# Kernel tuning notes

Measured on AMD Instinct MI355X. Metric: run time of the kernel, lower is better.

Reference implementation:

```python
import jax, jax.numpy as jnp
import numpy as np

H = 128
N_CAN = 100000
N_FLAG = 50000
E = 600000
L = 500000


def _sage_conv(x_src, x_dst, edge_index, Wl, bl, Wr):
    # PyG SAGEConv (mean aggr): lin_l(mean_{j in N(i)} x_j) + lin_r(x_i)
    src, dst = edge_index[0], edge_index[1]
    msg = x_src[src]                                        # [E, H] gather
    n_dst = x_dst.shape[0]
    agg = jax.ops.segment_sum(msg, dst, num_segments=n_dst)  # [N_dst, H]
    cnt = jax.ops.segment_sum(jnp.ones((msg.shape[0],), msg.dtype), dst,
                              num_segments=n_dst)
    mean = agg / jnp.maximum(cnt, 1.0)[:, None]
    return mean @ Wl.T + bl + x_dst @ Wr.T


def setup_inputs() -> dict:
    key = jax.random.key(0)
    ks = jax.random.split(key, 16)
    s = 1.0 / np.sqrt(H)
    inp = {
        'can_node_id': jnp.arange(N_CAN, dtype=jnp.int64) if jax.config.jax_enable_x64 else jnp.arange(N_CAN, dtype=jnp.int32),
        'flag_node_id': jnp.arange(N_FLAG, dtype=jnp.int32),
        'edge_index_cf': jnp.stack([
            jax.random.randint(ks[0], (E,), 0, N_CAN),
            jax.random.randint(ks[1], (E,), 0, N_FLAG)]),
        'edge_index_fc': jnp.stack([
            jax.random.randint(ks[2], (E,), 0, N_FLAG),
            jax.random.randint(ks[3], (E,), 0, N_CAN)]),
        'edge_label_index': jnp.stack([
            jax.random.randint(ks[4], (L,), 0, N_CAN),
            jax.random.randint(ks[5], (L,), 0, N_FLAG)]),
        'can_emb': jax.random.normal(ks[6], (N_CAN, H), jnp.float32),
        'flag_emb': jax.random.normal(ks[7], (N_FLAG, H), jnp.float32),
        # SAGEConv for edge type CAN->flag (updates flag nodes)
        'Wl_cf': jax.random.normal(ks[8], (H, H), jnp.float32) * s,
        'bl_cf': jnp.zeros((H,), jnp.float32),
        'Wr_cf': jax.random.normal(ks[9], (H, H), jnp.float32) * s,
        # SAGEConv for edge type flag->CAN (updates CAN nodes)
        'Wl_fc': jax.random.normal(ks[10], (H, H), jnp.float32) * s,
        'bl_fc': jnp.zeros((H,), jnp.float32),
        'Wr_fc': jax.random.normal(ks[11], (H, H), jnp.float32) * s,
        # classifier MLP
        'W1': jax.random.normal(ks[12], (H, 2 * H), jnp.float32) * (1.0 / np.sqrt(2 * H)),
        'b1': jnp.zeros((H,), jnp.float32),
        'W2': jax.random.normal(ks[13], (1, H), jnp.float32) * s,
        'b2': jnp.zeros((1,), jnp.float32),
    }
    return inp


def reference(can_node_id, flag_node_id, edge_index_cf, edge_index_fc,
              edge_label_index, can_emb, flag_emb,
              Wl_cf, bl_cf, Wr_cf, Wl_fc, bl_fc, Wr_fc,
              W1, b1, W2, b2):
    # embedding lookups
    x_can = can_emb[can_node_id]    # [N_CAN, H]
    x_flag = flag_emb[flag_node_id]  # [N_FLAG, H]
    # to_hetero single SAGE layer + relu (dropout is identity in eval)
    upd_flag = jax.nn.relu(_sage_conv(x_can, x_flag, edge_index_cf, Wl_cf, bl_cf, Wr_cf))
    upd_can = jax.nn.relu(_sage_conv(x_flag, x_can, edge_index_fc, Wl_fc, bl_fc, Wr_fc))
    # link prediction classifier
    src = upd_can[edge_label_index[0]]   # [L, H]
    dst = upd_flag[edge_label_index[1]]  # [L, H]
    h = jax.nn.relu(jnp.concatenate([src, dst], axis=-1) @ W1.T + b1)
    out = h @ W2.T + b2
    return out.reshape(-1)
```

## Files before the change

kernel.cpp:

```cpp
#include <hip/hip_runtime.h>
#include <hip/hip_bf16.h>

#define H 128
#define BSH 8
#define MAXB 1024

typedef __attribute__((ext_vector_type(8))) short short8;
typedef __attribute__((ext_vector_type(4))) short short4v;
typedef __attribute__((ext_vector_type(4))) float floatx4;
typedef unsigned short ushort_t;
typedef unsigned int uint_t;

__device__ __forceinline__ short f2bf(float f) {
    __hip_bfloat16 h = __float2bfloat16(f);
    return *reinterpret_cast<short*>(&h);
}
__device__ __forceinline__ float bflo(uint_t u) { return __uint_as_float(u << 16); }
__device__ __forceinline__ float bfhi(uint_t u) { return __uint_as_float(u & 0xFFFF0000u); }
__device__ __forceinline__ uint_t pack_bf2(float x, float y) {
    return (uint_t)(ushort_t)f2bf(x) | ((uint_t)(ushort_t)f2bf(y) << 16);
}

__global__ __launch_bounds__(256)
void bucket_hist_cvt_kernel(const int* __restrict__ ei1, const int* __restrict__ ei2,
                            int E, int NF, int B, int* __restrict__ bcnt, int nbh,
                            const float* __restrict__ a, int n4a,
                            const float* __restrict__ b, int n4b,
                            ushort_t* __restrict__ da, ushort_t* __restrict__ db,
                            const float* __restrict__ Wl_cf, const float* __restrict__ Wr_cf,
                            const float* __restrict__ Wl_fc, const float* __restrict__ Wr_fc,
                            const float* __restrict__ W1, ushort_t* __restrict__ wb) {
    __shared__ int h[MAXB];
    int tid = threadIdx.x;
    if ((int)blockIdx.x < nbh) {
        for (int i = tid; i < B; i += 256) h[i] = 0;
        __syncthreads();
        int base = blockIdx.x * 4096;
        #pragma unroll 4
        for (int it = 0; it < 16; ++it) {
            int t = base + it * 256 + tid;
            if (t < 2 * E) {
                int g = (t < E) ? ei1[E + t] : (ei2[E + t - E] + NF);
                atomicAdd(&h[g >> BSH], 1);
            }
        }
        __syncthreads();
        for (int i = tid; i < B; i += 256)
            if (h[i]) atomicAdd(&bcnt[i], h[i]);
        return;
    }
    int i = ((int)blockIdx.x - nbh) * 256 + tid;
    const float* src; ushort_t* dst; int k;
    if (i < n4a) { src = a; dst = da; k = i; }
    else if (i < n4a + n4b) { src = b; dst = db; k = i - n4a; }
    else {
        int idx = (i - n4a - n4b) * 4;
        if (idx >= 98304) return;
        int off;
        if      (idx < 16384) { src = Wl_cf; off = idx; }
        else if (idx < 32768) { src = Wr_cf; off = idx - 16384; }
        else if (idx < 49152) { src = Wl_fc; off = idx - 32768; }
        else if (idx < 65536) { src = Wr_fc; off = idx - 49152; }
        else                  { src = W1;    off = idx - 65536; }
        float4 v = *(const float4*)(src + off);
        short4v s;
        s[0] = f2bf(v.x); s[1] = f2bf(v.y); s[2] = f2bf(v.z); s[3] = f2bf(v.w);
        *(short4v*)(wb + idx) = s;
        return;
    }
    float4 v = ((const float4*)src)[k];
    short4v s;
    s[0] = f2bf(v.x); s[1] = f2bf(v.y); s[2] = f2bf(v.z); s[3] = f2bf(v.w);
    ((short4v*)dst)[k] = s;
}

__global__ __launch_bounds__(256)
void bucket_scan_kernel(const int* __restrict__ bcnt, int B,
                        int* __restrict__ bbase, int* __restrict__ bfront) {
    __shared__ int sdata[256];
    int tid = threadIdx.x;
    int base = tid * 4;
    int v[4]; int s = 0;
    #pragma unroll
    for (int i = 0; i < 4; ++i) { int idx = base + i; v[i] = (idx < B) ? bcnt[idx] : 0; s += v[i]; }
    sdata[tid] = s;
    __syncthreads();
    for (int off = 1; off < 256; off <<= 1) {
        int t = (tid >= off) ? sdata[tid - off] : 0;
        __syncthreads();
        sdata[tid] += t;
        __syncthreads();
    }
    int excl = tid ? sdata[tid - 1] : 0;
    #pragma unroll
    for (int i = 0; i < 4; ++i) {
        int idx = base + i;
        if (idx < B) { bbase[idx] = excl; bfront[idx] = excl; }
        excl += v[i];
    }
    if (tid == 255) bbase[B] = excl;
}

__global__ __launch_bounds__(256)
void partition_kernel(const int* __restrict__ ei1, const int* __restrict__ ei2,
                      int E, int NF, int B,
                      int* __restrict__ bfront, uint2* __restrict__ part) {
    __shared__ int h[MAXB];
    __shared__ int basex[MAXB];
    int tid = threadIdx.x;
    for (int i = tid; i < B; i += 256) h[i] = 0;
    __syncthreads();
    int base = blockIdx.x * 4096;
    #pragma unroll 4
    for (int it = 0; it < 16; ++it) {
        int t = base + it * 256 + tid;
        if (t < 2 * E) {
            int g = (t < E) ? ei1[E + t] : (ei2[E + t - E] + NF);
            atomicAdd(&h[g >> BSH], 1);
        }
    }
    __syncthreads();
    for (int i = tid; i < B; i += 256) {
        int c = h[i];
        basex[i] = c ? atomicAdd(&bfront[i], c) : 0;
    }
    __syncthreads();
    for (int i = tid; i < B; i += 256) h[i] = 0;
    __syncthreads();
    #pragma unroll 4
    for (int it = 0; it < 16; ++it) {
        int t = base + it * 256 + tid;
        if (t < 2 * E) {
            int g, s;
            if (t < E) { g = ei1[E + t]; s = ei1[t]; }
            else       { int e = t - E; g = ei2[E + e] + NF; s = ei2[e]; }
            int bk = g >> BSH;
            int r = atomicAdd(&h[bk], 1);
            part[basex[bk] + r] = make_uint2((uint_t)s, (uint_t)g);
        }
    }
}

__global__ __launch_bounds__(256)
void fine_bin_kernel(const int* __restrict__ bbase, int nTot,
                     const uint2* __restrict__ part,
                     int* __restrict__ offs, int* __restrict__ bins) {
    __shared__ int cnt[256];
    __shared__ int sdata[256];
    __shared__ int excl[256];
    int b = blockIdx.x;
    int tid = threadIdx.x;
    int seg0 = bbase[b], seg1 = bbase[b + 1];
    int gbase = b << BSH;
    cnt[tid] = 0;
    __syncthreads();
    for (int k = seg0 + tid; k < seg1; k += 256)
        atomicAdd(&cnt[part[k].y - gbase], 1);
    __syncthreads();
    sdata[tid] = cnt[tid];
    __syncthreads();
    for (int off = 1; off < 256; off <<= 1) {
        int t = (tid >= off) ? sdata[tid - off] : 0;
        __syncthreads();
        sdata[tid] += t;
        __syncthreads();
    }
    excl[tid] = tid ? sdata[tid - 1] : 0;
    int g = gbase + tid;
    if (g < nTot) offs[g] = seg0 + excl[tid];
    if (b == (int)gridDim.x - 1 && tid == 0) offs[nTot] = seg1;
    cnt[tid] = 0;
    __syncthreads();
    for (int k = seg0 + tid; k < seg1; k += 256) {
        uint2 e = part[k];
        int l = (int)e.y - gbase;
        int r = atomicAdd(&cnt[l], 1);
        bins[seg0 + excl[l] + r] = (int)e.x;
    }
}

__global__ __launch_bounds__(256)
void gather_mean3_kernel(const int* __restrict__ offs, int nTotal, int split,
                         const int* __restrict__ bins,
                         const ushort_t* __restrict__ embA, ushort_t* __restrict__ aggA,
                         const ushort_t* __restrict__ embB, ushort_t* __restrict__ aggB) {
    int g = blockIdx.x * 4 + (threadIdx.x >> 6);
    if (g >= nTotal) return;
    int lane = threadIdx.x & 63;
    int q = lane >> 4, l15 = lane & 15;
    int start = offs[g];
    int end = offs[g + 1];
    int deg = end - start;
    const ushort_t* emb; ushort_t* agg; int row;
    if (g < split) { emb = embA; agg = aggA; row = g; }
    else           { emb = embB; agg = aggB; row = g - split; }

    float acc[8];
    #pragma unroll
    for (int t = 0; t < 8; ++t) acc[t] = 0.f;

    int nPre = deg < 64 ? deg : 64;
    int pre = (lane < nPre) ? bins[start + lane] : 0;

    int col = l15 * 8;
    for (int it = 0; it < (nPre + 7) / 8; ++it) {
        int e0 = 8 * it + q;
        int e1 = e0 + 4;
        int s0 = __shfl(pre, e0, 64);
        int s1 = __shfl(pre, e1, 64);
        if (e0 < nPre) {
            uint4 r = *(const uint4*)(emb + (size_t)s0 * H + col);
            acc[0] += bflo(r.x); acc[1] += bfhi(r.x);
            acc[2] += bflo(r.y); acc[3] += bfhi(r.y);
            acc[4] += bflo(r.z); acc[5] += bfhi(r.z);
            acc[6] += bflo(r.w); acc[7] += bfhi(r.w);
        }
        if (e1 < nPre) {
            uint4 r = *(const uint4*)(emb + (size_t)s1 * H + col);
            acc[0] += bflo(r.x); acc[1] += bfhi(r.x);
            acc[2] += bflo(r.y); acc[3] += bfhi(r.y);
            acc[4] += bflo(r.z); acc[5] += bfhi(r.z);
            acc[6] += bflo(r.w); acc[7] += bfhi(r.w);
        }
    }
    for (int k = start + 64 + q; k < end; k += 4) {
        int s = bins[k];
        uint4 r = *(const uint4*)(emb + (size_t)s * H + col);
        acc[0] += bflo(r.x); acc[1] += bfhi(r.x);
        acc[2] += bflo(r.y); acc[3] += bfhi(r.y);
        acc[4] += bflo(r.z); acc[5] += bfhi(r.z);
        acc[6] += bflo(r.w); acc[7] += bfhi(r.w);
    }

    #pragma unroll
    for (int t = 0; t < 8; ++t) {
        acc[t] += __shfl_xor(acc[t], 16, 64);
        acc[t] += __shfl_xor(acc[t], 32, 64);
    }
    if (q == 0) {
        float inv = 1.0f / fmaxf((float)deg, 1.0f);
        uint4 o;
        o.x = pack_bf2(acc[0] * inv, acc[1] * inv);
        o.y = pack_bf2(acc[2] * inv, acc[3] * inv);
        o.z = pack_bf2(acc[4] * inv, acc[5] * inv);
        o.w = pack_bf2(acc[6] * inv, acc[7] * inv);
        *(uint4*)(agg + (size_t)row * H + col) = o;
    }
}

__global__ __launch_bounds__(256)
void hist2_kernel(const int* __restrict__ ei1, const int* __restrict__ ei2, int E,
                  int* __restrict__ deg1, int* __restrict__ deg2) {
    int t = blockIdx.x * 256 + threadIdx.x;
    if (t < E) atomicAdd(&deg1[ei1[E + t]], 1);
    else if (t < 2 * E) { int e = t - E; atomicAdd(&deg2[ei2[E + e]], 1); }
}

__global__ __launch_bounds__(256)
void scan_blocksum_kernel(const int* __restrict__ deg, int n, int* __restrict__ bsums) {
    __shared__ int sdata[256];
    int tid = threadIdx.x;
    int base = blockIdx.x * 1024 + tid * 4;
    int v = 0;
    #pragma unroll
    for (int i = 0; i < 4; ++i) { int idx = base + i; if (idx < n) v += deg[idx]; }
    sdata[tid] = v;
    __syncthreads();
    for (int off = 128; off > 0; off >>= 1) {
        if (tid < off) sdata[tid] += sdata[tid + off];
        __syncthreads();
    }
    if (tid == 0) bsums[blockIdx.x] = sdata[0];
}

__global__ __launch_bounds__(256)
void scan_write_kernel(int* __restrict__ data, int n, const int* __restrict__ bsums) {
    __shared__ int sdata[256];
    __shared__ int boff;
    int tid = threadIdx.x;
    if (tid < 64) {
        int acc = 0;
        for (int i = tid; i < (int)blockIdx.x; i += 64) acc += bsums[i];
        #pragma unroll
        for (int off = 32; off > 0; off >>= 1) acc += __shfl_xor(acc, off, 64);
        if (tid == 0) boff = acc;
    }
    int base = blockIdx.x * 1024 + tid * 4;
    int v[4]; int s = 0;
    #pragma unroll
    for (int i = 0; i < 4; ++i) { int idx = base + i; v[i] = (idx < n) ? data[idx] : 0; s += v[i]; }
    sdata[tid] = s;
    __syncthreads();
    for (int off = 1; off < 256; off <<= 1) {
        int t = (tid >= off) ? sdata[tid - off] : 0;
        __syncthreads();
        sdata[tid] += t;
        __syncthreads();
    }
    int excl = (tid == 0 ? 0 : sdata[tid - 1]) + boff;
    #pragma unroll
    for (int i = 0; i < 4; ++i) {
        int idx = base + i;
        if (idx < n) data[idx] = excl;
        excl += v[i];
    }
}

__global__ __launch_bounds__(256)
void bin2_kernel(const int* __restrict__ ei1, const int* __restrict__ ei2, int E,
                 int* __restrict__ offs1, int* __restrict__ offs2,
                 int* __restrict__ bins) {
    int t = blockIdx.x * 256 + threadIdx.x;
    if (t < E) {
        int pos = atomicAdd(&offs1[ei1[E + t]], 1);
        bins[pos] = ei1[t];
    } else if (t < 2 * E) {
        int e = t - E;
        int pos = atomicAdd(&offs2[ei2[E + e]], 1);
        bins[pos] = ei2[e];
    }
}

__global__ __launch_bounds__(256)
void gather_mean2_incl_kernel(const int* __restrict__ offs, int nTotal, int split,
                              const int* __restrict__ bins,
                              const ushort_t* __restrict__ embA, ushort_t* __restrict__ aggA,
                              const ushort_t* __restrict__ embB, ushort_t* __restrict__ aggB) {
    int g = blockIdx.x * 4 + (threadIdx.x >> 6);
    if (g >= nTotal) return;
    int lane = threadIdx.x & 63;
    int q = lane >> 4, l15 = lane & 15;
    int end = offs[g];
    int start = (g == 0) ? 0 : offs[g - 1];
    int deg = end - start;
    const ushort_t* emb; ushort_t* agg; int row;
    if (g < split) { emb = embA; agg = aggA; row = g; }
    else           { emb = embB; agg = aggB; row = g - split; }
    float acc[8];
    #pragma unroll
    for (int t = 0; t < 8; ++t) acc[t] = 0.f;
    int nPre = deg < 64 ? deg : 64;
    int pre = (lane < nPre) ? bins[start + lane] : 0;
    int col = l15 * 8;
    for (int it = 0; it < (nPre + 7) / 8; ++it) {
        int e0 = 8 * it + q, e1 = e0 + 4;
        int s0 = __shfl(pre, e0, 64);
        int s1 = __shfl(pre, e1, 64);
        if (e0 < nPre) {
            uint4 r = *(const uint4*)(emb + (size_t)s0 * H + col);
            acc[0] += bflo(r.x); acc[1] += bfhi(r.x);
            acc[2] += bflo(r.y); acc[3] += bfhi(r.y);
            acc[4] += bflo(r.z); acc[5] += bfhi(r.z);
            acc[6] += bflo(r.w); acc[7] += bfhi(r.w);
        }
        if (e1 < nPre) {
            uint4 r = *(const uint4*)(emb + (size_t)s1 * H + col);
            acc[0] += bflo(r.x); acc[1] += bfhi(r.x);
            acc[2] += bflo(r.y); acc[3] += bfhi(r.y);
            acc[4] += bflo(r.z); acc[5] += bfhi(r.z);
            acc[6] += bflo(r.w); acc[7] += bfhi(r.w);
        }
    }
    for (int k = start + 64 + q; k < end; k += 4) {
        int s = bins[k];
        uint4 r = *(const uint4*)(emb + (size_t)s * H + col);
        acc[0] += bflo(r.x); acc[1] += bfhi(r.x);
        acc[2] += bflo(r.y); acc[3] += bfhi(r.y);
        acc[4] += bflo(r.z); acc[5] += bfhi(r.z);
        acc[6] += bflo(r.w); acc[7] += bfhi(r.w);
    }
    #pragma unroll
    for (int t = 0; t < 8; ++t) {
        acc[t] += __shfl_xor(acc[t], 16, 64);
        acc[t] += __shfl_xor(acc[t], 32, 64);
    }
    if (q == 0) {
        float inv = 1.0f / fmaxf((float)deg, 1.0f);
        uint4 o;
        o.x = pack_bf2(acc[0] * inv, acc[1] * inv);
        o.y = pack_bf2(acc[2] * inv, acc[3] * inv);
        o.z = pack_bf2(acc[4] * inv, acc[5] * inv);
        o.w = pack_bf2(acc[6] * inv, acc[7] * inv);
        *(uint4*)(agg + (size_t)row * H + col) = o;
    }
}

__global__ __launch_bounds__(256)
void sage2_kernel(int nbF, int NF, int NC,
                  ushort_t* __restrict__ aggf, const ushort_t* __restrict__ embf,
                  ushort_t* __restrict__ aggc, const ushort_t* __restrict__ embc,
                  const ushort_t* __restrict__ wlf, const ushort_t* __restrict__ wrf,
                  const float* __restrict__ blf,
                  const ushort_t* __restrict__ wlc, const ushort_t* __restrict__ wrc,
                  const float* __restrict__ blc,
                  const ushort_t* __restrict__ W1) {
    __shared__ short A[64][264];
    bool isF = (int)blockIdx.x < nbF;
    int nrows = isF ? NF : NC;
    int rbase = (isF ? blockIdx.x : blockIdx.x - nbF) * 64;
    ushort_t* io = isF ? aggf : aggc;
    const ushort_t* emb = isF ? embf : embc;
    const ushort_t* Wl = isF ? wlf : wlc;
    const ushort_t* Wr = isF ? wrf : wrc;
    const float* bl = isF ? blf : blc;
    int koff = isF ? 128 : 0;

    int tid = threadIdx.x;
    int lane = tid & 63;
    int wv = tid >> 6;
    int l15 = lane & 15;
    int quad = lane >> 4;
    int nb0 = 32 * wv + l15;

    for (int idx = tid; idx < 64 * 64; idx += 256) {
        int r = idx >> 6, qq = idx & 63;
        int row = rbase + r;
        short4v s = (short4v){0, 0, 0, 0};
        if (row < nrows) {
            const ushort_t* src = (qq < 32) ? (io + (size_t)row * H + qq * 4)
                                            : (emb + (size_t)row * H + (qq - 32) * 4);
            s = *(const short4v*)src;
        }
        *(short4v*)&A[r][qq * 4] = s;
    }

    floatx4 acc[4][2];
    #pragma unroll
    for (int i = 0; i < 4; ++i)
        #pragma unroll
        for (int j = 0; j < 2; ++j)
            acc[i][j] = (floatx4){0.f, 0.f, 0.f, 0.f};

    float blv0 = bl[nb0];
    float blv1 = bl[nb0 + 16];
    __syncthreads();

    #pragma unroll
    for (int half = 0; half < 2; ++half) {
        const ushort_t* W = half ? Wr : Wl;
        #pragma unroll
        for (int ks = 0; ks < 4; ++ks) {
            int kb = ks * 32 + quad * 8;
            short8 b0 = *(const short8*)(W + (size_t)nb0 * H + kb);
            short8 b1 = *(const short8*)(W + (size_t)(nb0 + 16) * H + kb);
            int ka = half * 128 + kb;
            #pragma unroll
            for (int mt = 0; mt < 4; ++mt) {
                short8 a = *(const short8*)&A[16 * mt + l15][ka];
                acc[mt][0] = __builtin_amdgcn_mfma_f32_16x16x32_bf16(a, b0, acc[mt][0], 0, 0, 0);
                acc[mt][1] = __builtin_amdgcn_mfma_f32_16x16x32_bf16(a, b1, acc[mt][1], 0, 0, 0);
            }
        }
    }

    __syncthreads();
    #pragma unroll
    for (int mt = 0; mt < 4; ++mt)
        #pragma unroll
        for (int nt = 0; nt < 2; ++nt) {
            float blv = nt ? blv1 : blv0;
            int colw = nb0 + 16 * nt;
            #pragma unroll
            for (int rg = 0; rg < 4; ++rg) {
                int row = 16 * mt + quad * 4 + rg;
                A[row][colw] = f2bf(fmaxf(acc[mt][nt][rg] + blv, 0.0f));
                acc[mt][nt][rg] = 0.0f;
            }
        }
    __syncthreads();

    const ushort_t* W1p = W1 + koff;
    #pragma unroll
    for (int ks = 0; ks < 4; ++ks) {
        int kb = ks * 32 + quad * 8;
        short8 b0 = *(const short8*)(W1p + (size_t)nb0 * 256 + kb);
        short8 b1 = *(const short8*)(W1p + (size_t)(nb0 + 16) * 256 + kb);
        #pragma unroll
        for (int mt = 0; mt < 4; ++mt) {
            short8 a = *(const short8*)&A[16 * mt + l15][kb];
            acc[mt][0] = __builtin_amdgcn_mfma_f32_16x16x32_bf16(a, b0, acc[mt][0], 0, 0, 0);
            acc[mt][1] = __builtin_amdgcn_mfma_f32_16x16x32_bf16(a, b1, acc[mt][1], 0, 0, 0);
        }
    }

    #pragma unroll
    for (int mt = 0; mt < 4; ++mt)
        #pragma unroll
        for (int rg = 0; rg < 4; ++rg) {
            int row = rbase + 16 * mt + quad * 4 + rg;
            if (row < nrows) {
                io[(size_t)row * H + nb0]      = (ushort_t)f2bf(acc[mt][0][rg]);
                io[(size_t)row * H + nb0 + 16] = (ushort_t)f2bf(acc[mt][1][rg]);
            }
        }
}

__global__ __launch_bounds__(256)
void classify_kernel(const int* __restrict__ eli, int L,
                     const ushort_t* __restrict__ u_can,
                     const ushort_t* __restrict__ u_flag,
                     const float* __restrict__ b1,
                     const float* __restrict__ W2,
                     const float* __restrict__ b2,
                     float* __restrict__ out) {
    int tid = threadIdx.x;
    int lane = tid & 63;
    int wv = tid >> 6;
    int sub = lane >> 4;
    int l15 = lane & 15;
    int p = blockIdx.x * 16 + wv * 4 + sub;
    if (p >= L) return;
    int i = eli[p];
    int j = eli[L + p];
    uint4 a = ((const uint4*)(u_can  + (size_t)i * H))[l15];
    uint4 b = ((const uint4*)(u_flag + (size_t)j * H))[l15];
    float4 bb0 = ((const float4*)b1)[l15 * 2];
    float4 bb1 = ((const float4*)b1)[l15 * 2 + 1];
    float4 w0  = ((const float4*)W2)[l15 * 2];
    float4 w1  = ((const float4*)W2)[l15 * 2 + 1];
    float s = fmaxf(bflo(a.x) + bflo(b.x) + bb0.x, 0.f) * w0.x
            + fmaxf(bfhi(a.x) + bfhi(b.x) + bb0.y, 0.f) * w0.y
            + fmaxf(bflo(a.y) + bflo(b.y) + bb0.z, 0.f) * w0.z
            + fmaxf(bfhi(a.y) + bfhi(b.y) + bb0.w, 0.f) * w0.w
            + fmaxf(bflo(a.z) + bflo(b.z) + bb1.x, 0.f) * w1.x
            + fmaxf(bfhi(a.z) + bfhi(b.z) + bb1.y, 0.f) * w1.y
            + fmaxf(bflo(a.w) + bflo(b.w) + bb1.z, 0.f) * w1.z
            + fmaxf(bfhi(a.w) + bfhi(b.w) + bb1.w, 0.f) * w1.w;
    #pragma unroll
    for (int off = 8; off > 0; off >>= 1)
        s += __shfl_down(s, off, 16);
    if (l15 == 0) out[p] = s + b2[0];
}

extern "C" void kernel_launch(void* const* d_in, const int* in_sizes, int n_in,
                              void* d_out, int out_size, void* d_ws, size_t ws_size,
                              hipStream_t stream) {
    const int*   ei_cf    = (const int*)d_in[2];
    const int*   ei_fc    = (const int*)d_in[3];
    const int*   eli      = (const int*)d_in[4];
    const float* can_emb  = (const float*)d_in[5];
    const float* flag_emb = (const float*)d_in[6];
    const float* Wl_cf    = (const float*)d_in[7];
    const float* bl_cf    = (const float*)d_in[8];
    const float* Wr_cf    = (const float*)d_in[9];
    const float* Wl_fc    = (const float*)d_in[10];
    const float* bl_fc    = (const float*)d_in[11];
    const float* Wr_fc    = (const float*)d_in[12];
    const float* W1       = (const float*)d_in[13];
    const float* b1       = (const float*)d_in[14];
    const float* W2       = (const float*)d_in[15];
    const float* b2       = (const float*)d_in[16];
    float* out = (float*)d_out;

    const int NCAN  = in_sizes[0];
    const int NFLAG = in_sizes[1];
    const int E     = in_sizes[2] / 2;
    const int L     = in_sizes[4] / 2;
    const int nTot  = NCAN + NFLAG;
    const int B     = (nTot + 255) >> BSH;

    ushort_t* aggc = (ushort_t*)d_ws;
    ushort_t* aggf = aggc + (size_t)NCAN * H;
    ushort_t* embc = aggf + (size_t)NFLAG * H;
    ushort_t* embf = embc + (size_t)NCAN * H;
    char* tail = (char*)(embf + (size_t)NFLAG * H);
    size_t tail_off = (size_t)(tail - (char*)d_ws);

    int nbF = (NFLAG + 63) / 64, nbC = (NCAN + 63) / 64;
    int n4c = NCAN * H / 4, n4f = NFLAG * H / 4;
    int nbcvt = (n4c + n4f + 24576 + 255) / 256;

    size_t off_offs  = tail_off;
    size_t off_bcnt  = off_offs  + (size_t)(nTot + 1) * 4;
    size_t off_bbase = off_bcnt  + (size_t)MAXB * 4;
    size_t off_bfrnt = off_bbase + (size_t)(MAXB + 1) * 4;
    size_t off_bins  = off_bfrnt + (size_t)MAXB * 4;
    size_t off_part  = (off_bins + (size_t)2 * E * 4 + 7) & ~(size_t)7;
    size_t off_wb    = off_part + (size_t)2 * E * 8;
    size_t need_new  = off_wb + 98304 * 2;

    if (ws_size >= need_new && B <= MAXB) {
        int* offs   = (int*)((char*)d_ws + off_offs);
        int* bcnt   = (int*)((char*)d_ws + off_bcnt);
        int* bbase  = (int*)((char*)d_ws + off_bbase);
        int* bfront = (int*)((char*)d_ws + off_bfrnt);
        int* bins   = (int*)((char*)d_ws + off_bins);
        uint2* part = (uint2*)((char*)d_ws + off_part);
        ushort_t* wb = (ushort_t*)((char*)d_ws + off_wb);
        ushort_t* wb_wlcf = wb, *wb_wrcf = wb + 16384, *wb_wlfc = wb + 32768,
                 *wb_wrfc = wb + 49152, *wb_w1 = wb + 65536;

        int nbh = (2 * E + 4095) >> 12;
        hipMemsetAsync(bcnt, 0, (size_t)MAXB * 4, stream);
        bucket_hist_cvt_kernel<<<nbh + nbcvt, 256, 0, stream>>>(
            ei_cf, ei_fc, E, NFLAG, B, bcnt, nbh,
            can_emb, n4c, flag_emb, n4f, embc, embf,
            Wl_cf, Wr_cf, Wl_fc, Wr_fc, W1, wb);
        bucket_scan_kernel<<<1, 256, 0, stream>>>(bcnt, B, bbase, bfront);
        partition_kernel<<<nbh, 256, 0, stream>>>(ei_cf, ei_fc, E, NFLAG, B, bfront, part);
        fine_bin_kernel<<<B, 256, 0, stream>>>(bbase, nTot, part, offs, bins);
        gather_mean3_kernel<<<(nTot + 3) / 4, 256, 0, stream>>>(
            offs, nTot, NFLAG, bins, embc, aggf, embf, aggc);
        sage2_kernel<<<nbF + nbC, 256, 0, stream>>>(
            nbF, NFLAG, NCAN, aggf, embf, aggc, embc,
            wb_wlcf, wb_wrcf, bl_cf, wb_wlfc, wb_wrfc, bl_fc, wb_w1);
    } else {
        int* scanf_ = (int*)tail;
        int* scanc_ = scanf_ + NFLAG;
        int* bins   = scanc_ + NCAN;
        int* bsums  = bins + 2 * E;
        ushort_t* wb = (ushort_t*)(bsums + 256);
        ushort_t* wb_wlcf = wb, *wb_wrcf = wb + 16384, *wb_wlfc = wb + 32768,
                 *wb_wrfc = wb + 49152, *wb_w1 = wb + 65536;

        bucket_hist_cvt_kernel<<<nbcvt, 256, 0, stream>>>(
            ei_cf, ei_fc, E, NFLAG, B, (int*)tail , 0,
            can_emb, n4c, flag_emb, n4f, embc, embf,
            Wl_cf, Wr_cf, Wl_fc, Wr_fc, W1, wb);
        hipMemsetAsync(scanf_, 0, ((size_t)NFLAG + NCAN) * 4, stream);
        int nb = (nTot + 1023) / 1024;
        hist2_kernel<<<(2 * E + 255) / 256, 256, 0, stream>>>(ei_cf, ei_fc, E, scanf_, scanc_);
        scan_blocksum_kernel<<<nb, 256, 0, stream>>>(scanf_, nTot, bsums);
        scan_write_kernel<<<nb, 256, 0, stream>>>(scanf_, nTot, bsums);
        bin2_kernel<<<(2 * E + 255) / 256, 256, 0, stream>>>(ei_cf, ei_fc, E, scanf_, scanc_, bins);
        gather_mean2_incl_kernel<<<(nTot + 3) / 4, 256, 0, stream>>>(
            scanf_, nTot, NFLAG, bins, embc, aggf, embf, aggc);
        sage2_kernel<<<nbF + nbC, 256, 0, stream>>>(
            nbF, NFLAG, NCAN, aggf, embf, aggc, embc,
            wb_wlcf, wb_wrcf, bl_cf, wb_wlfc, wb_wrfc, bl_fc, wb_w1);
    }

    classify_kernel<<<(L + 15) / 16, 256, 0, stream>>>(
        eli, L, aggc, aggf, b1, W2, b2, out);
}
```

Baseline: 343.4 us.

## Fuse neighbor mean gather into SAGE GEMM kernel via shared memory tile

Merges the per-node mean aggregation kernel into the SAGE linear/MLP kernel. Each block now gathers neighbor means for its 64 rows directly into the shared-memory A tile, so the intermediate aggregation buffer is never written to and re-read from global memory, and one launch is removed. The cost is that each block has only 4 waves doing 16 serial gathers each, with 1/4 as many blocks as the old gather launch, which may leave less memory-level parallelism to hide the latency of random gathers. The fallback path gains a small kernel that converts inclusive offsets to start offsets.

```diff
diff --git a/kernel.cpp b/kernel.cpp
--- a/kernel.cpp
+++ b/kernel.cpp
@@ -180,72 +180,170 @@
 }
 
 __global__ __launch_bounds__(256)
-void gather_mean3_kernel(const int* __restrict__ offs, int nTotal, int split,
-                         const int* __restrict__ bins,
-                         const ushort_t* __restrict__ embA, ushort_t* __restrict__ aggA,
-                         const ushort_t* __restrict__ embB, ushort_t* __restrict__ aggB) {
-    int g = blockIdx.x * 4 + (threadIdx.x >> 6);
-    if (g >= nTotal) return;
-    int lane = threadIdx.x & 63;
-    int q = lane >> 4, l15 = lane & 15;
-    int start = offs[g];
-    int end = offs[g + 1];
-    int deg = end - start;
-    const ushort_t* emb; ushort_t* agg; int row;
-    if (g < split) { emb = embA; agg = aggA; row = g; }
-    else           { emb = embB; agg = aggB; row = g - split; }
-
-    float acc[8];
-    #pragma unroll
-    for (int t = 0; t < 8; ++t) acc[t] = 0.f;
-
-    int nPre = deg < 64 ? deg : 64;
-    int pre = (lane < nPre) ? bins[start + lane] : 0;
-
-    int col = l15 * 8;
-    for (int it = 0; it < (nPre + 7) / 8; ++it) {
-        int e0 = 8 * it + q;
-        int e1 = e0 + 4;
-        int s0 = __shfl(pre, e0, 64);
-        int s1 = __shfl(pre, e1, 64);
-        if (e0 < nPre) {
-            uint4 r = *(const uint4*)(emb + (size_t)s0 * H + col);
-            acc[0] += bflo(r.x); acc[1] += bfhi(r.x);
-            acc[2] += bflo(r.y); acc[3] += bfhi(r.y);
-            acc[4] += bflo(r.z); acc[5] += bfhi(r.z);
-            acc[6] += bflo(r.w); acc[7] += bfhi(r.w);
-        }
-        if (e1 < nPre) {
-            uint4 r = *(const uint4*)(emb + (size_t)s1 * H + col);
-            acc[0] += bflo(r.x); acc[1] += bfhi(r.x);
-            acc[2] += bflo(r.y); acc[3] += bfhi(r.y);
-            acc[4] += bflo(r.z); acc[5] += bfhi(r.z);
-            acc[6] += bflo(r.w); acc[7] += bfhi(r.w);
-        }
-    }
-    for (int k = start + 64 + q; k < end; k += 4) {
-        int s = bins[k];
-        uint4 r = *(const uint4*)(emb + (size_t)s * H + col);
-        acc[0] += bflo(r.x); acc[1] += bfhi(r.x);
-        acc[2] += bflo(r.y); acc[3] += bfhi(r.y);
-        acc[4] += bflo(r.z); acc[5] += bfhi(r.z);
-        acc[6] += bflo(r.w); acc[7] += bfhi(r.w);
-    }
-
-    #pragma unroll
-    for (int t = 0; t < 8; ++t) {
-        acc[t] += __shfl_xor(acc[t], 16, 64);
-        acc[t] += __shfl_xor(acc[t], 32, 64);
-    }
-    if (q == 0) {
-        float inv = 1.0f / fmaxf((float)deg, 1.0f);
-        uint4 o;
-        o.x = pack_bf2(acc[0] * inv, acc[1] * inv);
-        o.y = pack_bf2(acc[2] * inv, acc[3] * inv);
-        o.z = pack_bf2(acc[4] * inv, acc[5] * inv);
-        o.w = pack_bf2(acc[6] * inv, acc[7] * inv);
-        *(uint4*)(agg + (size_t)row * H + col) = o;
-    }
+void gather_sage_kernel(int nbF, int NF, int NC,
+                        const int* __restrict__ offs, const int* __restrict__ bins,
+                        ushort_t* __restrict__ uf, ushort_t* __restrict__ uc,
+                        const ushort_t* __restrict__ embf, const ushort_t* __restrict__ embc,
+                        const ushort_t* __restrict__ wlf, const ushort_t* __restrict__ wrf,
+                        const float* __restrict__ blf,
+                        const ushort_t* __restrict__ wlc, const ushort_t* __restrict__ wrc,
+                        const float* __restrict__ blc,
+                        const ushort_t* __restrict__ W1) {
+    __shared__ short A[64][264];
+    bool isF = (int)blockIdx.x < nbF;
+    int nrows = isF ? NF : NC;
+    int rbase = (isF ? blockIdx.x : blockIdx.x - nbF) * 64;
+    ushort_t* uo = isF ? uf : uc;
+    const ushort_t* embS = isF ? embf : embc;
+    const ushort_t* embN = isF ? embc : embf;
+    const ushort_t* Wl = isF ? wlf : wlc;
+    const ushort_t* Wr = isF ? wrf : wrc;
+    const float* bl = isF ? blf : blc;
+    int goff = isF ? 0 : NF;
+    int koff = isF ? 128 : 0;
+
+    int tid = threadIdx.x;
+    int lane = tid & 63;
+    int wv = tid >> 6;
+    int l15 = lane & 15;
+    int quad = lane >> 4;
+    int col8 = l15 * 8;
+    int nb0 = 32 * wv + l15;
+
+    for (int rr = 0; rr < 16; ++rr) {
+        int r = wv * 16 + rr;
+        int row = rbase + r;
+        float acc[8];
+        #pragma unroll
+        for (int t = 0; t < 8; ++t) acc[t] = 0.f;
+        int deg = 0;
+        if (row < nrows) {
+            int g = goff + row;
+            int start = offs[g];
+            int end = offs[g + 1];
+            deg = end - start;
+            int nPre = deg < 64 ? deg : 64;
+            int pre = (lane < nPre) ? bins[start + lane] : 0;
+            for (int it = 0; it < (nPre + 7) / 8; ++it) {
+                int e0 = 8 * it + quad;
+                int e1 = e0 + 4;
+                int s0 = __shfl(pre, e0, 64);
+                int s1 = __shfl(pre, e1, 64);
+                if (e0 < nPre) {
+                    uint4 rv = *(const uint4*)(embN + (size_t)s0 * H + col8);
+                    acc[0] += bflo(rv.x); acc[1] += bfhi(rv.x);
+                    acc[2] += bflo(rv.y); acc[3] += bfhi(rv.y);
+                    acc[4] += bflo(rv.z); acc[5] += bfhi(rv.z);
+                    acc[6] += bflo(rv.w); acc[7] += bfhi(rv.w);
+                }
+                if (e1 < nPre) {
+                    uint4 rv = *(const uint4*)(embN + (size_t)s1 * H + col8);
+                    acc[0] += bflo(rv.x); acc[1] += bfhi(rv.x);
+                    acc[2] += bflo(rv.y); acc[3] += bfhi(rv.y);
+                    acc[4] += bflo(rv.z); acc[5] += bfhi(rv.z);
+                    acc[6] += bflo(rv.w); acc[7] += bfhi(rv.w);
+                }
+            }
+            for (int k = start + 64 + quad; k < end; k += 4) {
+                int s = bins[k];
+                uint4 rv = *(const uint4*)(embN + (size_t)s * H + col8);
+                acc[0] += bflo(rv.x); acc[1] += bfhi(rv.x);
+                acc[2] += bflo(rv.y); acc[3] += bfhi(rv.y);
+                acc[4] += bflo(rv.z); acc[5] += bfhi(rv.z);
+                acc[6] += bflo(rv.w); acc[7] += bfhi(rv.w);
+            }
+        }
+        #pragma unroll
+        for (int t = 0; t < 8; ++t) {
+            acc[t] += __shfl_xor(acc[t], 16, 64);
+            acc[t] += __shfl_xor(acc[t], 32, 64);
+        }
+        if (quad == 0) {
+            float inv = 1.0f / fmaxf((float)deg, 1.0f);
+            short8 o;
+            #pragma unroll
+            for (int t = 0; t < 8; ++t) o[t] = f2bf(acc[t] * inv);
+            *(short8*)&A[r][col8] = o;
+        }
+    }
+
+    for (int idx = tid; idx < 64 * 32; idx += 256) {
+        int r = idx >> 5, qq = idx & 31;
+        int row = rbase + r;
+        short4v s = (short4v){0, 0, 0, 0};
+        if (row < nrows) s = *(const short4v*)(embS + (size_t)row * H + qq * 4);
+        *(short4v*)&A[r][128 + qq * 4] = s;
+    }
+
+    floatx4 acc[4][2];
+    #pragma unroll
+    for (int i = 0; i < 4; ++i)
+        #pragma unroll
+        for (int j = 0; j < 2; ++j)
+            acc[i][j] = (floatx4){0.f, 0.f, 0.f, 0.f};
+
+    float blv0 = bl[nb0];
+    float blv1 = bl[nb0 + 16];
+    __syncthreads();
+
+    #pragma unroll
+    for (int half = 0; half < 2; ++half) {
+        const ushort_t* W = half ? Wr : Wl;
+        #pragma unroll
+        for (int ks = 0; ks < 4; ++ks) {
+            int kb = ks * 32 + quad * 8;
+            short8 b0 = *(const short8*)(W + (size_t)nb0 * H + kb);
+            short8 b1 = *(const short8*)(W + (size_t)(nb0 + 16) * H + kb);
+            int ka = half * 128 + kb;
+            #pragma unroll
+            for (int mt = 0; mt < 4; ++mt) {
+                short8 a = *(const short8*)&A[16 * mt + l15][ka];
+                acc[mt][0] = __builtin_amdgcn_mfma_f32_16x16x32_bf16(a, b0, acc[mt][0], 0, 0, 0);
+                acc[mt][1] = __builtin_amdgcn_mfma_f32_16x16x32_bf16(a, b1, acc[mt][1], 0, 0, 0);
+            }
+        }
+    }
+
+    __syncthreads();
+    #pragma unroll
+    for (int mt = 0; mt < 4; ++mt)
+        #pragma unroll
+        for (int nt = 0; nt < 2; ++nt) {
+            float blv = nt ? blv1 : blv0;
+            int colw = nb0 + 16 * nt;
+            #pragma unroll
+            for (int rg = 0; rg < 4; ++rg) {
+                int row = 16 * mt + quad * 4 + rg;
+                A[row][colw] = f2bf(fmaxf(acc[mt][nt][rg] + blv, 0.0f));
+                acc[mt][nt][rg] = 0.0f;
+            }
+        }
+    __syncthreads();
+
+    const ushort_t* W1p = W1 + koff;
+    #pragma unroll
+    for (int ks = 0; ks < 4; ++ks) {
+        int kb = ks * 32 + quad * 8;
+        short8 b0 = *(const short8*)(W1p + (size_t)nb0 * 256 + kb);
+        short8 b1 = *(const short8*)(W1p + (size_t)(nb0 + 16) * 256 + kb);
+        #pragma unroll
+        for (int mt = 0; mt < 4; ++mt) {
+            short8 a = *(const short8*)&A[16 * mt + l15][kb];
+            acc[mt][0] = __builtin_amdgcn_mfma_f32_16x16x32_bf16(a, b0, acc[mt][0], 0, 0, 0);
+            acc[mt][1] = __builtin_amdgcn_mfma_f32_16x16x32_bf16(a, b1, acc[mt][1], 0, 0, 0);
+        }
+    }
+
+    #pragma unroll
+    for (int mt = 0; mt < 4; ++mt)
+        #pragma unroll
+        for (int rg = 0; rg < 4; ++rg) {
+            int row = rbase + 16 * mt + quad * 4 + rg;
+            if (row < nrows) {
+                uo[(size_t)row * H + nb0]      = (ushort_t)f2bf(acc[mt][0][rg]);
+                uo[(size_t)row * H + nb0 + 16] = (ushort_t)f2bf(acc[mt][1][rg]);
+            }
+        }
 }
 
 __global__ __launch_bounds__(256)
@@ -304,6 +402,13 @@
         if (idx < n) data[idx] = excl;
         excl += v[i];
     }
+}
+
+__global__ __launch_bounds__(256)
+void incl_to_start_kernel(const int* __restrict__ incl, int nTot, int* __restrict__ offs) {
+    int g = blockIdx.x * 256 + threadIdx.x;
+    if (g < nTot) offs[g + 1] = incl[g];
+    if (g == 0) offs[0] = 0;
 }
 
 __global__ __launch_bounds__(256)
@@ -319,180 +424,6 @@
         int pos = atomicAdd(&offs2[ei2[E + e]], 1);
         bins[pos] = ei2[e];
     }
-}
-
-__global__ __launch_bounds__(256)
-void gather_mean2_incl_kernel(const int* __restrict__ offs, int nTotal, int split,
-                              const int* __restrict__ bins,
-                              const ushort_t* __restrict__ embA, ushort_t* __restrict__ aggA,
-                              const ushort_t* __restrict__ embB, ushort_t* __restrict__ aggB) {
-    int g = blockIdx.x * 4 + (threadIdx.x >> 6);
-    if (g >= nTotal) return;
-    int lane = threadIdx.x & 63;
-    int q = lane >> 4, l15 = lane & 15;
-    int end = offs[g];
-    int start = (g == 0) ? 0 : offs[g - 1];
-    int deg = end - start;
-    const ushort_t* emb; ushort_t* agg; int row;
-    if (g < split) { emb = embA; agg = aggA; row = g; }
-    else           { emb = embB; agg = aggB; row = g - split; }
-    float acc[8];
-    #pragma unroll
-    for (int t = 0; t < 8; ++t) acc[t] = 0.f;
-    int nPre = deg < 64 ? deg : 64;
-    int pre = (lane < nPre) ? bins[start + lane] : 0;
-    int col = l15 * 8;
-    for (int it = 0; it < (nPre + 7) / 8; ++it) {
-        int e0 = 8 * it + q, e1 = e0 + 4;
-        int s0 = __shfl(pre, e0, 64);
-        int s1 = __shfl(pre, e1, 64);
-        if (e0 < nPre) {
-            uint4 r = *(const uint4*)(emb + (size_t)s0 * H + col);
-            acc[0] += bflo(r.x); acc[1] += bfhi(r.x);
-            acc[2] += bflo(r.y); acc[3] += bfhi(r.y);
-            acc[4] += bflo(r.z); acc[5] += bfhi(r.z);
-            acc[6] += bflo(r.w); acc[7] += bfhi(r.w);
-        }
-        if (e1 < nPre) {
-            uint4 r = *(const uint4*)(emb + (size_t)s1 * H + col);
-            acc[0] += bflo(r.x); acc[1] += bfhi(r.x);
-            acc[2] += bflo(r.y); acc[3] += bfhi(r.y);
-            acc[4] += bflo(r.z); acc[5] += bfhi(r.z);
-            acc[6] += bflo(r.w); acc[7] += bfhi(r.w);
-        }
-    }
-    for (int k = start + 64 + q; k < end; k += 4) {
-        int s = bins[k];
-        uint4 r = *(const uint4*)(emb + (size_t)s * H + col);
-        acc[0] += bflo(r.x); acc[1] += bfhi(r.x);
-        acc[2] += bflo(r.y); acc[3] += bfhi(r.y);
-        acc[4] += bflo(r.z); acc[5] += bfhi(r.z);
-        acc[6] += bflo(r.w); acc[7] += bfhi(r.w);
-    }
-    #pragma unroll
-    for (int t = 0; t < 8; ++t) {
-        acc[t] += __shfl_xor(acc[t], 16, 64);
-        acc[t] += __shfl_xor(acc[t], 32, 64);
-    }
-    if (q == 0) {
-        float inv = 1.0f / fmaxf((float)deg, 1.0f);
-        uint4 o;
-        o.x = pack_bf2(acc[0] * inv, acc[1] * inv);
-        o.y = pack_bf2(acc[2] * inv, acc[3] * inv);
-        o.z = pack_bf2(acc[4] * inv, acc[5] * inv);
-        o.w = pack_bf2(acc[6] * inv, acc[7] * inv);
-        *(uint4*)(agg + (size_t)row * H + col) = o;
-    }
-}
-
-__global__ __launch_bounds__(256)
-void sage2_kernel(int nbF, int NF, int NC,
-                  ushort_t* __restrict__ aggf, const ushort_t* __restrict__ embf,
-                  ushort_t* __restrict__ aggc, const ushort_t* __restrict__ embc,
-                  const ushort_t* __restrict__ wlf, const ushort_t* __restrict__ wrf,
-                  const float* __restrict__ blf,
-                  const ushort_t* __restrict__ wlc, const ushort_t* __restrict__ wrc,
-                  const float* __restrict__ blc,
-                  const ushort_t* __restrict__ W1) {
-    __shared__ short A[64][264];
-    bool isF = (int)blockIdx.x < nbF;
-    int nrows = isF ? NF : NC;
-    int rbase = (isF ? blockIdx.x : blockIdx.x - nbF) * 64;
-    ushort_t* io = isF ? aggf : aggc;
-    const ushort_t* emb = isF ? embf : embc;
-    const ushort_t* Wl = isF ? wlf : wlc;
-    const ushort_t* Wr = isF ? wrf : wrc;
-    const float* bl = isF ? blf : blc;
-    int koff = isF ? 128 : 0;
-
-    int tid = threadIdx.x;
-    int lane = tid & 63;
-    int wv = tid >> 6;
-    int l15 = lane & 15;
-    int quad = lane >> 4;
-    int nb0 = 32 * wv + l15;
-
-    for (int idx = tid; idx < 64 * 64; idx += 256) {
-        int r = idx >> 6, qq = idx & 63;
-        int row = rbase + r;
-        short4v s = (short4v){0, 0, 0, 0};
-        if (row < nrows) {
-            const ushort_t* src = (qq < 32) ? (io + (size_t)row * H + qq * 4)
-                                            : (emb + (size_t)row * H + (qq - 32) * 4);
-            s = *(const short4v*)src;
-        }
-        *(short4v*)&A[r][qq * 4] = s;
-    }
-
-    floatx4 acc[4][2];
-    #pragma unroll
-    for (int i = 0; i < 4; ++i)
-        #pragma unroll
-        for (int j = 0; j < 2; ++j)
-            acc[i][j] = (floatx4){0.f, 0.f, 0.f, 0.f};
-
-    float blv0 = bl[nb0];
-    float blv1 = bl[nb0 + 16];
-    __syncthreads();
-
-    #pragma unroll
-    for (int half = 0; half < 2; ++half) {
-        const ushort_t* W = half ? Wr : Wl;
-        #pragma unroll
-        for (int ks = 0; ks < 4; ++ks) {
-            int kb = ks * 32 + quad * 8;
-            short8 b0 = *(const short8*)(W + (size_t)nb0 * H + kb);
-            short8 b1 = *(const short8*)(W + (size_t)(nb0 + 16) * H + kb);
-            int ka = half * 128 + kb;
-            #pragma unroll
-            for (int mt = 0; mt < 4; ++mt) {
-                short8 a = *(const short8*)&A[16 * mt + l15][ka];
-                acc[mt][0] = __builtin_amdgcn_mfma_f32_16x16x32_bf16(a, b0, acc[mt][0], 0, 0, 0);
-                acc[mt][1] = __builtin_amdgcn_mfma_f32_16x16x32_bf16(a, b1, acc[mt][1], 0, 0, 0);
-            }
-        }
-    }
-
-    __syncthreads();
-    #pragma unroll
-    for (int mt = 0; mt < 4; ++mt)
-        #pragma unroll
-        for (int nt = 0; nt < 2; ++nt) {
-            float blv = nt ? blv1 : blv0;
-            int colw = nb0 + 16 * nt;
-            #pragma unroll
-            for (int rg = 0; rg < 4; ++rg) {
-                int row = 16 * mt + quad * 4 + rg;
-                A[row][colw] = f2bf(fmaxf(acc[mt][nt][rg] + blv, 0.0f));
-                acc[mt][nt][rg] = 0.0f;
-            }
-        }
-    __syncthreads();
-
-    const ushort_t* W1p = W1 + koff;
-    #pragma unroll
-    for (int ks = 0; ks < 4; ++ks) {
-        int kb = ks * 32 + quad * 8;
-        short8 b0 = *(const short8*)(W1p + (size_t)nb0 * 256 + kb);
-        short8 b1 = *(const short8*)(W1p + (size_t)(nb0 + 16) * 256 + kb);
-        #pragma unroll
-        for (int mt = 0; mt < 4; ++mt) {
-            short8 a = *(const short8*)&A[16 * mt + l15][kb];
-            acc[mt][0] = __builtin_amdgcn_mfma_f32_16x16x32_bf16(a, b0, acc[mt][0], 0, 0, 0);
-            acc[mt][1] = __builtin_amdgcn_mfma_f32_16x16x32_bf16(a, b1, acc[mt][1], 0, 0, 0);
-        }
-    }
-
-    #pragma unroll
-    for (int mt = 0; mt < 4; ++mt)
-        #pragma unroll
-        for (int rg = 0; rg < 4; ++rg) {
-            int row = rbase + 16 * mt + quad * 4 + rg;
-            if (row < nrows) {
-                io[(size_t)row * H + nb0]      = (ushort_t)f2bf(acc[mt][0][rg]);
-                io[(size_t)row * H + nb0 + 16] = (ushort_t)f2bf(acc[mt][1][rg]);
-            }
-        }
 }
 
 __global__ __launch_bounds__(256)
@@ -559,9 +490,9 @@
     const int nTot  = NCAN + NFLAG;
     const int B     = (nTot + 255) >> BSH;
 
-    ushort_t* aggc = (ushort_t*)d_ws;
-    ushort_t* aggf = aggc + (size_t)NCAN * H;
-    ushort_t* embc = aggf + (size_t)NFLAG * H;
+    ushort_t* uc   = (ushort_t*)d_ws;
+    ushort_t* uf   = uc + (size_t)NCAN * H;
+    ushort_t* embc = uf + (size_t)NFLAG * H;
     ushort_t* embf = embc + (size_t)NCAN * H;
     char* tail = (char*)(embf + (size_t)NFLAG * H);
     size_t tail_off = (size_t)(tail - (char*)d_ws);
@@ -579,12 +510,13 @@
     size_t off_wb    = off_part + (size_t)2 * E * 8;
     size_t need_new  = off_wb + 98304 * 2;
 
+    int* offs   = (int*)((char*)d_ws + off_offs);
+    int* bcnt   = (int*)((char*)d_ws + off_bcnt);
+    int* bbase  = (int*)((char*)d_ws + off_bbase);
+    int* bfront = (int*)((char*)d_ws + off_bfrnt);
+    int* bins   = (int*)((char*)d_ws + off_bins);
+
     if (ws_size >= need_new && B <= MAXB) {
-        int* offs   = (int*)((char*)d_ws + off_offs);
-        int* bcnt   = (int*)((char*)d_ws + off_bcnt);
-        int* bbase  = (int*)((char*)d_ws + off_bbase);
-        int* bfront = (int*)((char*)d_ws + off_bfrnt);
-        int* bins   = (int*)((char*)d_ws + off_bins);
         uint2* part = (uint2*)((char*)d_ws + off_part);
         ushort_t* wb = (ushort_t*)((char*)d_ws + off_wb);
         ushort_t* wb_wlcf = wb, *wb_wrcf = wb + 16384, *wb_wlfc = wb + 32768,
@@ -599,22 +531,20 @@
         bucket_scan_kernel<<<1, 256, 0, stream>>>(bcnt, B, bbase, bfront);
         partition_kernel<<<nbh, 256, 0, stream>>>(ei_cf, ei_fc, E, NFLAG, B, bfront, part);
         fine_bin_kernel<<<B, 256, 0, stream>>>(bbase, nTot, part, offs, bins);
-        gather_mean3_kernel<<<(nTot + 3) / 4, 256, 0, stream>>>(
-            offs, nTot, NFLAG, bins, embc, aggf, embf, aggc);
-        sage2_kernel<<<nbF + nbC, 256, 0, stream>>>(
-            nbF, NFLAG, NCAN, aggf, embf, aggc, embc,
+        gather_sage_kernel<<<nbF + nbC, 256, 0, stream>>>(
+            nbF, NFLAG, NCAN, offs, bins, uf, uc, embf, embc,
             wb_wlcf, wb_wrcf, bl_cf, wb_wlfc, wb_wrfc, bl_fc, wb_w1);
     } else {
-        int* scanf_ = (int*)tail;
+        int* scanf_ = bins;
         int* scanc_ = scanf_ + NFLAG;
-        int* bins   = scanc_ + NCAN;
-        int* bsums  = bins + 2 * E;
+        int* bins2  = scanc_ + NCAN;
+        int* bsums  = bins2 + 2 * E;
         ushort_t* wb = (ushort_t*)(bsums + 256);
         ushort_t* wb_wlcf = wb, *wb_wrcf = wb + 16384, *wb_wlfc = wb + 32768,
                  *wb_wrfc = wb + 49152, *wb_w1 = wb + 65536;
 
         bucket_hist_cvt_kernel<<<nbcvt, 256, 0, stream>>>(
-            ei_cf, ei_fc, E, NFLAG, B, (int*)tail , 0,
+            ei_cf, ei_fc, E, NFLAG, B, bcnt, 0,
             can_emb, n4c, flag_emb, n4f, embc, embf,
             Wl_cf, Wr_cf, Wl_fc, Wr_fc, W1, wb);
         hipMemsetAsync(scanf_, 0, ((size_t)NFLAG + NCAN) * 4, stream);
@@ -622,14 +552,13 @@
         hist2_kernel<<<(2 * E + 255) / 256, 256, 0, stream>>>(ei_cf, ei_fc, E, scanf_, scanc_);
         scan_blocksum_kernel<<<nb, 256, 0, stream>>>(scanf_, nTot, bsums);
         scan_write_kernel<<<nb, 256, 0, stream>>>(scanf_, nTot, bsums);
-        bin2_kernel<<<(2 * E + 255) / 256, 256, 0, stream>>>(ei_cf, ei_fc, E, scanf_, scanc_, bins);
-        gather_mean2_incl_kernel<<<(nTot + 3) / 4, 256, 0, stream>>>(
-            scanf_, nTot, NFLAG, bins, embc, aggf, embf, aggc);
-        sage2_kernel<<<nbF + nbC, 256, 0, stream>>>(
-            nbF, NFLAG, NCAN, aggf, embf, aggc, embc,
+        bin2_kernel<<<(2 * E + 255) / 256, 256, 0, stream>>>(ei_cf, ei_fc, E, scanf_, scanc_, bins2);
+        incl_to_start_kernel<<<(nTot + 255) / 256, 256, 0, stream>>>(scanf_, nTot, offs);
+        gather_sage_kernel<<<nbF + nbC, 256, 0, stream>>>(
+            nbF, NFLAG, NCAN, offs, bins2, uf, uc, embf, embc,
             wb_wlcf, wb_wrcf, bl_cf, wb_wlfc, wb_wrfc, bl_fc, wb_w1);
     }
 
     classify_kernel<<<(L + 15) / 16, 256, 0, stream>>>(
-        eli, L, aggc, aggf, b1, W2, b2, out);
-}
+        eli, L, uc, uf, b1, W2, b2, out);
+}
```

After: 356.9 us. 3.9% more time.
